# Kernel tuning notes

Measured on AMD Instinct MI355X. Metric: run time of the kernel, lower is better.

## Reference

```python
import jax, jax.numpy as jnp
import numpy as np

N = 50000      # nodes
E = 800000     # edges
D = 256        # num_feat == num_hidden == out_dim
G = 64         # graphs in batch
C = 64         # num_classes
L = 2          # cells (layers)
S = 2          # GNN steps per cell
SCALE = 0.05


def setup_inputs() -> dict:
    key = jax.random.key(0)
    ks = jax.random.split(key, 10)
    x = jax.random.normal(ks[0], (N, D), jnp.float32)
    edge_index = jax.random.randint(ks[1], (2, E), 0, N, dtype=jnp.int64)
    edge_attr = jax.random.normal(ks[2], (E, 1), jnp.float32)
    batch = jnp.sort(jax.random.randint(ks[3], (N,), 0, G, dtype=jnp.int64))
    pre_w = jax.random.normal(ks[4], (L, 2, D, D), jnp.float32) * SCALE
    pre_b = jax.random.normal(ks[5], (L, 2, D), jnp.float32) * SCALE
    gcn_w = jax.random.normal(ks[6], (L, S, D, D), jnp.float32) * SCALE
    gcn_b = jax.random.normal(ks[7], (L, S, D), jnp.float32) * SCALE
    cls_w = jax.random.normal(ks[8], (D, C), jnp.float32) * SCALE
    cls_b = jax.random.normal(ks[9], (C,), jnp.float32) * SCALE
    return {"x": x, "edge_index": edge_index, "edge_attr": edge_attr,
            "batch": batch, "pre_w": pre_w, "pre_b": pre_b,
            "gcn_w": gcn_w, "gcn_b": gcn_b, "cls_w": cls_w, "cls_b": cls_b}


def reference(x, edge_index, edge_attr, batch, pre_w, pre_b, gcn_w, gcn_b, cls_w, cls_b):
    n = x.shape[0]
    # GCNConv with self-loops and symmetric normalization (torch_geometric default)
    loops = jnp.arange(n, dtype=edge_index.dtype)
    src = jnp.concatenate([edge_index[0], loops])   # [E+N]
    dst = jnp.concatenate([edge_index[1], loops])   # [E+N]
    deg = jax.ops.segment_sum(jnp.ones_like(dst, dtype=x.dtype), dst, num_segments=n)
    dinv = jax.lax.rsqrt(deg)                        # deg >= 1 due to self loops
    norm = (dinv[src] * dinv[dst])[:, None]          # [E+N, 1]

    def gcn(h, w, b):
        hw = h @ w                                   # [N, D]
        msg = hw[src] * norm                         # gather + scale
        return jax.ops.segment_sum(msg, dst, num_segments=n) + b

    def cell(s0, s1, l):
        s0 = s0 @ pre_w[l, 0] + pre_b[l, 0]
        s1 = s1 @ pre_w[l, 1] + pre_b[l, 1]
        states = [s0, s1]
        for i, idx in enumerate((0, 1)):             # NAS indices [0, 1]
            states.append(gcn(states[idx], gcn_w[l, i], gcn_b[l, i]))
        # concat='add': tmp = states[2]; then accumulate states[2:] again
        tmp = states[2]
        for st in states[2:]:
            tmp = tmp + st                           # = 2*s2 + s3 (faithful)
        return tmp

    s0 = s1 = x
    for l in range(L):
        s0, s1 = s1, cell(s0, s1, l)
    out = s1                                         # [N, D]

    g = cls_b.shape[0] if False else G
    counts = jax.ops.segment_sum(jnp.ones((n,), x.dtype), batch, num_segments=G)
    mean_pool = jax.ops.segment_sum(out, batch, num_segments=G) / jnp.maximum(counts, 1.0)[:, None]
    max_pool = jax.ops.segment_max(out, batch, num_segments=G)
    max_pool = jnp.where(counts[:, None] > 0, max_pool, 0.0)
    pooled = mean_pool + max_pool                    # [G, D]
    return pooled @ cls_w + cls_b                    # [G, C]
```

## Files before the change

### kernel.cpp

```cpp
#include <hip/hip_runtime.h>

typedef __attribute__((ext_vector_type(8))) short bf16x8;
typedef __attribute__((ext_vector_type(4))) float f32x4;

__device__ inline float bf2f(unsigned short u) {
    union { float f; unsigned int i; } v; v.i = ((unsigned int)u) << 16; return v.f;
}
__device__ inline unsigned short f2bf(float f) {
    union { float f; unsigned int u; } v; v.f = f;
    unsigned int x = v.u;
    unsigned int r = x + 0x7FFFu + ((x >> 16) & 1u);
    return (unsigned short)(r >> 16);
}
__device__ inline unsigned int fenc(float x) {
    union { float f; unsigned int u; } v; v.f = x;
    return (v.u & 0x80000000u) ? ~v.u : (v.u | 0x80000000u);
}
__device__ inline float fdec(unsigned int k) {
    union { float f; unsigned int u; } v;
    v.u = (k & 0x80000000u) ? (k & 0x7FFFFFFFu) : ~k;
    return v.f;
}
__device__ inline float ldf(const void* p, size_t i, int f32) {
    return f32 ? ((const float*)p)[i] : bf2f(((const unsigned short*)p)[i]);
}
__device__ inline int ldi(const int* p, size_t i, int i64) {
    return i64 ? p[2 * i] : p[i];
}

__global__ __launch_bounds__(256)
void k_detect(const unsigned short* __restrict__ xu, int xstride,
              const int* __restrict__ ei, int estride, int* __restrict__ flags) {
    __shared__ int cnt, orv;
    if (threadIdx.x == 0) { cnt = 0; orv = 0; }
    __syncthreads();
    int c = 0, o = 0;
    for (int s = 0; s < 4; ++s) {
        int j = threadIdx.x * 4 + s;
        size_t k = (size_t)j * xstride;
        unsigned short u = xu[2 * k];
        int e = (u >> 7) & 0xFF;
        if (e >= 100 && e <= 140) ++c;
        size_t idx = (size_t)j * estride;
        o |= ei[2 * idx + 1];
    }
    atomicAdd(&cnt, c); atomicOr(&orv, o);
    __syncthreads();
    if (threadIdx.x == 0) {
        flags[0] = (cnt < 768) ? 1 : 0;
        flags[1] = (orv == 0) ? 1 : 0;
    }
}

__global__ void k_zero(int* __restrict__ hist, int* __restrict__ cursor,
                       float* __restrict__ psum, unsigned int* __restrict__ pkey,
                       int* __restrict__ pcnt, int N) {
    int t = blockIdx.x * 256 + threadIdx.x;
    if (t < N) hist[t] = 0;
    else if (t < 2 * N) cursor[t - N] = 0;
    else if (t < 2 * N + 16384) psum[t - 2 * N] = 0.f;
    else if (t < 2 * N + 32768) pkey[t - 2 * N - 16384] = 0u;
    else if (t < 2 * N + 32768 + 64) pcnt[t - 2 * N - 32768] = 0;
}

__global__ __launch_bounds__(256)
void k_cvt(const void* __restrict__ X, unsigned short* __restrict__ Xb,
           size_t nelem, const int* __restrict__ flags) {
    int f = flags[0];
    size_t i = ((size_t)blockIdx.x * 256 + threadIdx.x) * 8;
    if (i >= nelem) return;
    if (f) {
        const float* s = (const float*)X + i;
        float4 f0 = *(const float4*)s;
        float4 f1 = *(const float4*)(s + 4);
        int4 o;
        o.x = (int)f2bf(f0.x) | ((int)f2bf(f0.y) << 16);
        o.y = (int)f2bf(f0.z) | ((int)f2bf(f0.w) << 16);
        o.z = (int)f2bf(f1.x) | ((int)f2bf(f1.y) << 16);
        o.w = (int)f2bf(f1.z) | ((int)f2bf(f1.w) << 16);
        *(int4*)(Xb + i) = o;
    } else {
        *(int4*)(Xb + i) = *(const int4*)((const unsigned short*)X + i);
    }
}

__global__ __launch_bounds__(256)
void k_cvtw(const void* __restrict__ pre_w, const void* __restrict__ gcn_w,
            unsigned short* __restrict__ Pb, unsigned short* __restrict__ Gt,
            const int* __restrict__ flags) {
    __shared__ float tile[64][65];
    const int i = blockIdx.y;
    const int m0 = (blockIdx.x & 3) * 64;
    const int n0 = (blockIdx.x >> 2) * 64;
    const int f = flags[0];
    const size_t base = (size_t)i * 65536;
#pragma unroll
    for (int q = 0; q < 16; ++q) {
        int idx = q * 256 + threadIdx.x;
        int r = idx >> 6, c = idx & 63;
        size_t src = base + (size_t)(m0 + r) * 256 + n0 + c;
        Pb[src] = f2bf(ldf(pre_w, src, f));
        tile[r][c] = ldf(gcn_w, src, f);
    }
    __syncthreads();
#pragma unroll
    for (int q = 0; q < 16; ++q) {
        int idx = q * 256 + threadIdx.x;
        int r = idx >> 6, c = idx & 63;
        Gt[base + (size_t)(n0 + r) * 256 + m0 + c] = f2bf(tile[c][r]);
    }
}

__global__ __launch_bounds__(256)
void k_prepw(const unsigned short* __restrict__ Pb, const unsigned short* __restrict__ Gt,
             unsigned short* __restrict__ Wt0, unsigned short* __restrict__ Wt1) {
    const int which = blockIdx.y;
    const int wid = threadIdx.x >> 6, lane = threadIdx.x & 63;
    const int tile = blockIdx.x * 4 + wid;
    const int n0 = (tile >> 4) * 16, k0 = (tile & 15) * 16;
    const int l15 = lane & 15, hi = lane >> 4;
    size_t base0, base1 = 0;
    if (which == 0)      { base0 = 0; base1 = 65536; }
    else if (which == 1) { base0 = 2 * 65536; }
    else                 { base0 = 3 * 65536; }
    f32x4 acc0 = {}, acc1 = {};
    const unsigned short* ga = Gt + base0 + (size_t)(n0 + l15) * 256 + hi * 8;
    const unsigned short* pa = Pb + base0 + (size_t)(k0 + l15) * 256 + hi * 8;
    const unsigned short* gb = Gt + base1 + (size_t)(n0 + l15) * 256 + hi * 8;
    const unsigned short* pb = Pb + base1 + (size_t)(k0 + l15) * 256 + hi * 8;
#pragma unroll
    for (int kt = 0; kt < 8; ++kt) {
        bf16x8 a0 = *(const bf16x8*)(ga + kt * 32);
        bf16x8 b0 = *(const bf16x8*)(pa + kt * 32);
        acc0 = __builtin_amdgcn_mfma_f32_16x16x32_bf16(a0, b0, acc0, 0, 0, 0);
        if (which == 0) {
            bf16x8 a1 = *(const bf16x8*)(gb + kt * 32);
            bf16x8 b1 = *(const bf16x8*)(pb + kt * 32);
            acc1 = __builtin_amdgcn_mfma_f32_16x16x32_bf16(a1, b1, acc1, 0, 0, 0);
        }
    }
#pragma unroll
    for (int j = 0; j < 4; ++j) {
        int n = n0 + hi * 4 + j;
        int k = k0 + l15;
        if (which == 0)      Wt0[(size_t)n * 256 + k]       = f2bf(2.f * acc0[j] + acc1[j]);
        else if (which == 1) Wt1[(size_t)n * 512 + k]       = f2bf(2.f * acc0[j]);
        else                 Wt1[(size_t)n * 512 + 256 + k] = f2bf(acc0[j]);
    }
}

__global__ __launch_bounds__(256)
void k_prepb(const void* __restrict__ pre_b, const unsigned short* __restrict__ Gt,
             const void* __restrict__ gcn_b,
             float* __restrict__ cvec, float* __restrict__ dvec,
             const int* __restrict__ flags) {
    __shared__ float pb[2][256];
    const int l = blockIdx.x, n = threadIdx.x;
    const int f = flags[0];
    pb[0][n] = ldf(pre_b, (size_t)(l * 2 + 0) * 256 + n, f);
    pb[1][n] = ldf(pre_b, (size_t)(l * 2 + 1) * 256 + n, f);
    __syncthreads();
    const unsigned short* g0 = Gt + (size_t)(l * 2 + 0) * 65536 + (size_t)n * 256;
    const unsigned short* g1 = Gt + (size_t)(l * 2 + 1) * 65536 + (size_t)n * 256;
    float a = 0.f, b = 0.f;
#pragma unroll 4
    for (int mc = 0; mc < 32; ++mc) {
        bf16x8 v0 = *(const bf16x8*)(g0 + mc * 8);
        bf16x8 v1 = *(const bf16x8*)(g1 + mc * 8);
#pragma unroll
        for (int u = 0; u < 8; ++u) {
            a += pb[0][mc * 8 + u] * bf2f((unsigned short)v0[u]);
            b += pb[1][mc * 8 + u] * bf2f((unsigned short)v1[u]);
        }
    }
    cvec[l * 256 + n] = 2.f * a + b;
    dvec[l * 256 + n] = 2.f * ldf(gcn_b, (size_t)(l * 2 + 0) * 256 + n, f)
                            + ldf(gcn_b, (size_t)(l * 2 + 1) * 256 + n, f);
}

__global__ void k_hist(const int* __restrict__ ei, int E, int N,
                       int* __restrict__ hist, const int* __restrict__ flags) {
    int e = blockIdx.x * 256 + threadIdx.x;
    if (e >= E) return;
    int i64 = flags[1];
    int d = ldi(ei, (size_t)E + e, i64); d = d < 0 ? 0 : (d >= N ? N - 1 : d);
    atomicAdd(&hist[d], 1);
}

__global__ __launch_bounds__(256)
void k_scan1(const int* __restrict__ hist, int* __restrict__ pre,
             int* __restrict__ bsum, int N) {
    __shared__ int s[256];
    int i = blockIdx.x * 256 + threadIdx.x;
    int v = (i < N) ? hist[i] : 0;
    s[threadIdx.x] = v;
    __syncthreads();
    for (int off = 1; off < 256; off <<= 1) {
        int t = (threadIdx.x >= off) ? s[threadIdx.x - off] : 0;
        __syncthreads();
        s[threadIdx.x] += t;
        __syncthreads();
    }
    if (i < N) pre[i] = s[threadIdx.x] - v;
    if (threadIdx.x == 255) bsum[blockIdx.x] = s[255];
}

__global__ __launch_bounds__(256)
void k_scan2(const int* __restrict__ bsum, int* __restrict__ boff,
             int* __restrict__ rowptr, int nb, int N) {
    __shared__ int s[256];
    int t = threadIdx.x;
    int v = (t < nb) ? bsum[t] : 0;
    s[t] = v;
    __syncthreads();
    for (int off = 1; off < 256; off <<= 1) {
        int x = (t >= off) ? s[t - off] : 0;
        __syncthreads();
        s[t] += x;
        __syncthreads();
    }
    if (t < nb) boff[t] = s[t] - v;
    if (t == nb - 1) rowptr[N] = s[t];
}

__global__ __launch_bounds__(256)
void k_scan3(const int* __restrict__ hist, const int* __restrict__ pre,
             const int* __restrict__ boff, int* __restrict__ rowptr,
             float* __restrict__ dinv, int N) {
    int i = blockIdx.x * 256 + threadIdx.x;
    if (i < N) {
        rowptr[i] = pre[i] + boff[blockIdx.x];
        dinv[i] = rsqrtf((float)(hist[i] + 1));
    }
}

__global__ void k_scatter(const int* __restrict__ ei, int E, int N,
                          const int* __restrict__ rowptr, int* __restrict__ cursor,
                          int* __restrict__ col, const int* __restrict__ flags) {
    int e = blockIdx.x * 256 + threadIdx.x;
    if (e >= E) return;
    int i64 = flags[1];
    int s = ldi(ei, (size_t)e, i64);     s = s < 0 ? 0 : (s >= N ? N - 1 : s);
    int d = ldi(ei, (size_t)E + e, i64); d = d < 0 ? 0 : (d >= N ? N - 1 : d);
    int pos = rowptr[d] + atomicAdd(&cursor[d], 1);
    col[pos] = s;
}

__global__ __launch_bounds__(512)
void k_gemm(const unsigned short* __restrict__ Xb, const unsigned short* __restrict__ Yb,
            const unsigned short* __restrict__ Wt, const float* __restrict__ cvec,
            const float* __restrict__ dinv, unsigned short* __restrict__ out,
            int M, int K) {
    __shared__ char ldsb[49152];
    const int tid = threadIdx.x;
    const int lane = tid & 63;
    const int wid = tid >> 6;
    const int wm = wid >> 2, wn = wid & 3;
    const int l15 = lane & 15, hi = lane >> 4;
    const int row0 = blockIdx.x * 128;

    f32x4 acc[4][4] = {};
    const int KT = K / 64;
    for (int kt = 0; kt < KT; ++kt) {
        const int k0 = kt * 64;
        const unsigned short* Asrc = (k0 < 256) ? Xb : Yb;
        const int ak0 = (k0 < 256) ? k0 : k0 - 256;
        int4 ra[2], rw[4];
#pragma unroll
        for (int q = 0; q < 2; ++q) {
            int id = q * 512 + tid;
            int r = id >> 3, cb = id & 7;
            int grow = row0 + r; if (grow > M - 1) grow = M - 1;
            ra[q] = *(const int4*)(Asrc + (size_t)grow * 256 + ak0 + cb * 8);
        }
#pragma unroll
        for (int q = 0; q < 4; ++q) {
            int id = q * 512 + tid;
            int r = id >> 3, cb = id & 7;
            rw[q] = *(const int4*)(Wt + (size_t)r * K + k0 + cb * 8);
        }
        __syncthreads();
#pragma unroll
        for (int q = 0; q < 2; ++q) {
            int id = q * 512 + tid;
            int r = id >> 3, cb = id & 7;
            int sw = (cb * 16) ^ ((r & 7) << 4);
            *(int4*)(ldsb + r * 128 + sw) = ra[q];
        }
#pragma unroll
        for (int q = 0; q < 4; ++q) {
            int id = q * 512 + tid;
            int r = id >> 3, cb = id & 7;
            int sw = (cb * 16) ^ ((r & 7) << 4);
            *(int4*)(ldsb + 16384 + r * 128 + sw) = rw[q];
        }
        __syncthreads();
#pragma unroll
        for (int kk = 0; kk < 2; ++kk) {
            bf16x8 af[4], bfr[4];
            int byte = kk * 64 + (hi << 4);
#pragma unroll
            for (int m = 0; m < 4; ++m) {
                int r = wm * 64 + m * 16 + l15;
                af[m] = *(const bf16x8*)(ldsb + r * 128 + (byte ^ ((r & 7) << 4)));
            }
#pragma unroll
            for (int n = 0; n < 4; ++n) {
                int r = wn * 64 + n * 16 + l15;
                bfr[n] = *(const bf16x8*)(ldsb + 16384 + r * 128 + (byte ^ ((r & 7) << 4)));
            }
#pragma unroll
            for (int m = 0; m < 4; ++m)
#pragma unroll
                for (int n = 0; n < 4; ++n)
                    acc[m][n] = __builtin_amdgcn_mfma_f32_16x16x32_bf16(af[m], bfr[n], acc[m][n], 0, 0, 0);
        }
    }
    for (int half = 0; half < 2; ++half) {
        __syncthreads();
        if (wm == half) {
#pragma unroll
            for (int m = 0; m < 4; ++m) {
#pragma unroll
                for (int j = 0; j < 4; ++j) {
                    int rl = m * 16 + hi * 4 + j;
                    int grow = row0 + half * 64 + rl;
                    if (grow < M) {
                        float di = dinv[grow];
#pragma unroll
                        for (int n = 0; n < 4; ++n) {
                            int colc = wn * 64 + n * 16 + l15;
                            float v = (acc[m][n][j] + cvec[colc]) * di;
                            *(unsigned short*)(ldsb + rl * 512 + colc * 2) = f2bf(v);
                        }
                    }
                }
            }
        }
        __syncthreads();
#pragma unroll
        for (int p = 0; p < 4; ++p) {
            int rl = p * 16 + (tid >> 5);
            int cb = tid & 31;
            int grow = row0 + half * 64 + rl;
            if (grow < M)
                *(int4*)(out + (size_t)grow * 256 + cb * 8) = *(const int4*)(ldsb + rl * 512 + cb * 16);
        }
    }
}

__global__ __launch_bounds__(256)
void k_agg(const unsigned short* __restrict__ U, const int* __restrict__ rowptr,
           const int* __restrict__ col, const float* __restrict__ dinv,
           const float* __restrict__ dvec, unsigned short* __restrict__ Y, int N) {
    int w = (blockIdx.x * 256 + threadIdx.x) >> 6;
    int lane = threadIdx.x & 63;
    if (w >= N) return;
    const size_t loff = (size_t)lane * 4;
    ushort4 sv = *(const ushort4*)(U + (size_t)w * 256 + loff);
    float a0 = bf2f(sv.x), a1 = bf2f(sv.y), a2 = bf2f(sv.z), a3 = bf2f(sv.w);
    int beg = rowptr[w], end = rowptr[w + 1];
    int e = beg;
    for (; e + 16 <= end; e += 16) {
        int s[16];
        ushort4 v[16];
#pragma unroll
        for (int u = 0; u < 16; ++u) s[u] = __builtin_amdgcn_readfirstlane(col[e + u]);
#pragma unroll
        for (int u = 0; u < 16; ++u) v[u] = *(const ushort4*)(U + (size_t)s[u] * 256 + loff);
#pragma unroll
        for (int u = 0; u < 16; ++u) {
            a0 += bf2f(v[u].x); a1 += bf2f(v[u].y);
            a2 += bf2f(v[u].z); a3 += bf2f(v[u].w);
        }
    }
    for (; e + 4 <= end; e += 4) {
        int s[4];
        ushort4 v[4];
#pragma unroll
        for (int u = 0; u < 4; ++u) s[u] = __builtin_amdgcn_readfirstlane(col[e + u]);
#pragma unroll
        for (int u = 0; u < 4; ++u) v[u] = *(const ushort4*)(U + (size_t)s[u] * 256 + loff);
#pragma unroll
        for (int u = 0; u < 4; ++u) {
            a0 += bf2f(v[u].x); a1 += bf2f(v[u].y);
            a2 += bf2f(v[u].z); a3 += bf2f(v[u].w);
        }
    }
    for (; e < end; ++e) {
        int s = __builtin_amdgcn_readfirstlane(col[e]);
        ushort4 v = *(const ushort4*)(U + (size_t)s * 256 + loff);
        a0 += bf2f(v.x); a1 += bf2f(v.y); a2 += bf2f(v.z); a3 += bf2f(v.w);
    }
    float di = dinv[w];
    int f = lane * 4;
    a0 = a0 * di + dvec[f + 0];
    a1 = a1 * di + dvec[f + 1];
    a2 = a2 * di + dvec[f + 2];
    a3 = a3 * di + dvec[f + 3];
    ushort4 o; o.x = f2bf(a0); o.y = f2bf(a1); o.z = f2bf(a2); o.w = f2bf(a3);
    *(ushort4*)(Y + (size_t)w * 256 + loff) = o;
}

__global__ __launch_bounds__(256)
void k_pool(const unsigned short* __restrict__ Y, const int* __restrict__ batch, int N,
            float* __restrict__ psum, unsigned int* __restrict__ pkey, int* __restrict__ pcnt,
            const int* __restrict__ flags) {
    int f = threadIdx.x;
    int base = blockIdx.x * 64;
    if (base >= N) return;
    int i64 = flags[1];
    int g0 = ldi(batch, base, i64); int curg = g0 < 0 ? 0 : (g0 > 63 ? 63 : g0);
    float s = 0.f, mx = -__builtin_inff(); int cnt = 0;
#pragma unroll 4
    for (int r = 0; r < 64; ++r) {
        int node = base + r;
        if (node >= N) break;
        int g = ldi(batch, node, i64); g = g < 0 ? 0 : (g > 63 ? 63 : g);
        if (g != curg) {
            atomicAdd(&psum[curg * 256 + f], s);
            atomicMax(&pkey[curg * 256 + f], fenc(mx));
            if (f == 0) atomicAdd(&pcnt[curg], cnt);
            curg = g; s = 0.f; mx = -__builtin_inff(); cnt = 0;
        }
        float v = bf2f(Y[(size_t)node * 256 + f]);
        s += v; mx = fmaxf(mx, v); ++cnt;
    }
    atomicAdd(&psum[curg * 256 + f], s);
    atomicMax(&pkey[curg * 256 + f], fenc(mx));
    if (f == 0) atomicAdd(&pcnt[curg], cnt);
}

__global__ __launch_bounds__(64)
void k_cls(const float* __restrict__ psum, const unsigned int* __restrict__ pkey,
           const int* __restrict__ pcnt, const void* __restrict__ clsw,
           const void* __restrict__ clsb, float* __restrict__ outf,
           unsigned short* __restrict__ outu, const int* __restrict__ flags) {
    __shared__ float pooled[256];
    int g = blockIdx.x, c = threadIdx.x;
    int f = flags[0];
    int cnt = pcnt[g];
    for (int m = c; m < 256; m += 64) {
        float mean = psum[g * 256 + m] / (float)(cnt > 0 ? cnt : 1);
        float mx = (cnt > 0) ? fdec(pkey[g * 256 + m]) : 0.f;
        pooled[m] = mean + mx;
    }
    __syncthreads();
    float a = ldf(clsb, c, f);
#pragma unroll 8
    for (int m = 0; m < 256; ++m) a += pooled[m] * ldf(clsw, (size_t)m * 64 + c, f);
    if (f) outf[g * 64 + c] = a;
    else   outu[g * 64 + c] = f2bf(a);
}

extern "C" void kernel_launch(void* const* d_in, const int* in_sizes, int n_in,
                              void* d_out, int out_size, void* d_ws, size_t ws_size,
                              hipStream_t stream) {
    const void*           X     = d_in[0];
    const int*            EI    = (const int*)d_in[1];
    const int*            BATCH = (const int*)d_in[3];
    const void*           PREW  = d_in[4];
    const void*           PREB  = d_in[5];
    const void*           GCNW  = d_in[6];
    const void*           GCNB  = d_in[7];
    const void*           CLSW  = d_in[8];
    const void*           CLSB  = d_in[9];

    const int N = in_sizes[3];
    const int E = in_sizes[1] / 2;
    const int NB = (N + 255) / 256;

    char* ws = (char*)d_ws;
    size_t off = 0;
    auto alloc = [&](size_t b) { size_t o = off; off += (b + 255) & ~(size_t)255; return o; };
    int*            flags  = (int*)(ws + alloc(256));
    float*          dinv   = (float*)(ws + alloc((size_t)N * 4));
    int*            hist   = (int*)(ws + alloc((size_t)N * 4));
    int*            cursor = (int*)(ws + alloc((size_t)N * 4));
    int*            rowptr = (int*)(ws + alloc((size_t)(N + 1) * 4));
    int*            pre    = (int*)(ws + alloc((size_t)N * 4));
    int*            bsum   = (int*)(ws + alloc((size_t)NB * 4));
    int*            boff   = (int*)(ws + alloc((size_t)NB * 4));
    int*            col    = (int*)(ws + alloc((size_t)E * 4));
    unsigned short* Pb     = (unsigned short*)(ws + alloc(4 * 65536 * 2));
    unsigned short* Gt     = (unsigned short*)(ws + alloc(4 * 65536 * 2));
    unsigned short* Wt0    = (unsigned short*)(ws + alloc(256 * 256 * 2));
    unsigned short* Wt1    = (unsigned short*)(ws + alloc(256 * 512 * 2));
    float*          cvec   = (float*)(ws + alloc(512 * 4));
    float*          dvec   = (float*)(ws + alloc(512 * 4));
    float*          psum   = (float*)(ws + alloc(64 * 256 * 4));
    unsigned int*   pkey   = (unsigned int*)(ws + alloc(64 * 256 * 4));
    int*            pcnt   = (int*)(ws + alloc(64 * 4));
    unsigned short* Xb     = (unsigned short*)(ws + alloc((size_t)N * 256 * 2));
    unsigned short* U      = (unsigned short*)(ws + alloc((size_t)N * 256 * 2));
    unsigned short* Y      = (unsigned short*)(ws + alloc((size_t)N * 256 * 2));

    int zt = 2 * N + 32768 + 64;
    k_zero<<<(zt + 255) / 256, 256, 0, stream>>>(hist, cursor, psum, pkey, pcnt, N);

    int xstride = (in_sizes[0] / 2) / 1024; if (xstride < 1) xstride = 1;
    int estride = E / 1024;                 if (estride < 1) estride = 1;
    k_detect<<<1, 256, 0, stream>>>((const unsigned short*)X, xstride, EI, estride, flags);

    size_t xelem = (size_t)N * 256;
    k_cvt<<<(int)((xelem / 8 + 255) / 256), 256, 0, stream>>>(X, Xb, xelem, flags);

    k_hist<<<(E + 255) / 256, 256, 0, stream>>>(EI, E, N, hist, flags);
    k_scan1<<<NB, 256, 0, stream>>>(hist, pre, bsum, N);
    k_scan2<<<1, 256, 0, stream>>>(bsum, boff, rowptr, NB, N);
    k_scan3<<<NB, 256, 0, stream>>>(hist, pre, boff, rowptr, dinv, N);
    k_scatter<<<(E + 255) / 256, 256, 0, stream>>>(EI, E, N, rowptr, cursor, col, flags);

    k_cvtw<<<dim3(16, 4), 256, 0, stream>>>(PREW, GCNW, Pb, Gt, flags);
    k_prepw<<<dim3(64, 3), 256, 0, stream>>>(Pb, Gt, Wt0, Wt1);
    k_prepb<<<2, 256, 0, stream>>>(PREB, Gt, GCNB, cvec, dvec, flags);

    int ggrid = (N + 127) / 128;
    k_gemm<<<ggrid, 512, 0, stream>>>(Xb, U, Wt0, cvec, dinv, U, N, 256);
    k_agg<<<(N + 3) / 4, 256, 0, stream>>>(U, rowptr, col, dinv, dvec, Y, N);
    k_gemm<<<ggrid, 512, 0, stream>>>(Xb, Y, Wt1, cvec + 256, dinv, U, N, 512);
    k_agg<<<(N + 3) / 4, 256, 0, stream>>>(U, rowptr, col, dinv, dvec + 256, Y, N);
    k_pool<<<(N + 63) / 64, 256, 0, stream>>>(Y, BATCH, N, psum, pkey, pcnt, flags);
    k_cls<<<64, 64, 0, stream>>>(psum, pkey, pcnt, CLSW, CLSB,
                                 (float*)d_out, (unsigned short*)d_out, flags);
}
```

Baseline: 403.5 us.

## Load GEMM MFMA fragments directly from global memory, bypassing LDS staging

The GEMM kernel no longer stages A and W tiles through shared memory with swizzled stores and two barriers per k-tile. Each wave now reads its MFMA operand fragments straight from global memory using precomputed row offsets, and the LDS buffer is shrunk since it is only used by the epilogue. This removes the barriers and LDS traffic, but every wave re-fetches data that was shared before, and the 16-byte per-lane loads are strided across rows. The kernel therefore leans on L1/L2 caching for reuse, which may raise memory traffic and latency.

```diff
diff --git a/kernel.cpp b/kernel.cpp
--- a/kernel.cpp
+++ b/kernel.cpp
@@ -251,7 +251,7 @@
             const unsigned short* __restrict__ Wt, const float* __restrict__ cvec,
             const float* __restrict__ dinv, unsigned short* __restrict__ out,
             int M, int K) {
-    __shared__ char ldsb[49152];
+    __shared__ char ldsb[32768];
     const int tid = threadIdx.x;
     const int lane = tid & 63;
     const int wid = tid >> 6;
@@ -259,56 +259,32 @@
     const int l15 = lane & 15, hi = lane >> 4;
     const int row0 = blockIdx.x * 128;
 
+    size_t aoff[4], woff[4];
+#pragma unroll
+    for (int m = 0; m < 4; ++m) {
+        int r = row0 + wm * 64 + m * 16 + l15;
+        if (r > M - 1) r = M - 1;
+        aoff[m] = (size_t)r * 256 + hi * 8;
+    }
+#pragma unroll
+    for (int n = 0; n < 4; ++n)
+        woff[n] = (size_t)(wn * 64 + n * 16 + l15) * K + hi * 8;
+
     f32x4 acc[4][4] = {};
     const int KT = K / 64;
     for (int kt = 0; kt < KT; ++kt) {
         const int k0 = kt * 64;
         const unsigned short* Asrc = (k0 < 256) ? Xb : Yb;
         const int ak0 = (k0 < 256) ? k0 : k0 - 256;
-        int4 ra[2], rw[4];
-#pragma unroll
-        for (int q = 0; q < 2; ++q) {
-            int id = q * 512 + tid;
-            int r = id >> 3, cb = id & 7;
-            int grow = row0 + r; if (grow > M - 1) grow = M - 1;
-            ra[q] = *(const int4*)(Asrc + (size_t)grow * 256 + ak0 + cb * 8);
-        }
-#pragma unroll
-        for (int q = 0; q < 4; ++q) {
-            int id = q * 512 + tid;
-            int r = id >> 3, cb = id & 7;
-            rw[q] = *(const int4*)(Wt + (size_t)r * K + k0 + cb * 8);
-        }
-        __syncthreads();
-#pragma unroll
-        for (int q = 0; q < 2; ++q) {
-            int id = q * 512 + tid;
-            int r = id >> 3, cb = id & 7;
-            int sw = (cb * 16) ^ ((r & 7) << 4);
-            *(int4*)(ldsb + r * 128 + sw) = ra[q];
-        }
-#pragma unroll
-        for (int q = 0; q < 4; ++q) {
-            int id = q * 512 + tid;
-            int r = id >> 3, cb = id & 7;
-            int sw = (cb * 16) ^ ((r & 7) << 4);
-            *(int4*)(ldsb + 16384 + r * 128 + sw) = rw[q];
-        }
-        __syncthreads();
 #pragma unroll
         for (int kk = 0; kk < 2; ++kk) {
             bf16x8 af[4], bfr[4];
-            int byte = kk * 64 + (hi << 4);
-#pragma unroll
-            for (int m = 0; m < 4; ++m) {
-                int r = wm * 64 + m * 16 + l15;
-                af[m] = *(const bf16x8*)(ldsb + r * 128 + (byte ^ ((r & 7) << 4)));
-            }
-#pragma unroll
-            for (int n = 0; n < 4; ++n) {
-                int r = wn * 64 + n * 16 + l15;
-                bfr[n] = *(const bf16x8*)(ldsb + 16384 + r * 128 + (byte ^ ((r & 7) << 4)));
-            }
+#pragma unroll
+            for (int m = 0; m < 4; ++m)
+                af[m] = *(const bf16x8*)(Asrc + aoff[m] + ak0 + kk * 32);
+#pragma unroll
+            for (int n = 0; n < 4; ++n)
+                bfr[n] = *(const bf16x8*)(Wt + woff[n] + k0 + kk * 32);
 #pragma unroll
             for (int m = 0; m < 4; ++m)
 #pragma unroll
```

After: 411.2 us. About the same (+1.9%).
